# Kernel tuning notes

Measured on AMD Instinct MI355X. Metric: run time of the kernel, lower is better.

The kernel has to match this reference:

```python
import jax, jax.numpy as jnp
import numpy as np

S, T, H, D = 4096, 4096, 16, 64
N_EMBD = H * D

def setup_inputs() -> dict:
    key = jax.random.key(0)
    kq, kk, kv, kw = jax.random.split(key, 4)
    q = jax.random.normal(kq, (S, H, D), dtype=jnp.float32)
    k = jax.random.normal(kk, (T, H, D), dtype=jnp.float32)
    v = jax.random.normal(kv, (T, H, D), dtype=jnp.float32)
    # GPT-2 style init: std = 0.02 / sqrt(2 * n_layer), n_layer = 24
    W_proj = jax.random.normal(kw, (N_EMBD, N_EMBD), dtype=jnp.float32) * (0.02 / np.sqrt(2 * 24))
    return {"q": q, "k": k, "v": v, "W_proj": W_proj}

def reference(q, k, v, W_proj):
    s, h, d = q.shape
    t = k.shape[0]
    # causal bias: mask positions where query index < key index (future keys)
    causal_bias = (jnp.arange(s)[:, None] < jnp.arange(t)[None, :]).astype(jnp.float32) * -10000.0
    scale = 1.0 / jnp.sqrt(jnp.float32(d))
    # [h, s, t] scores in fp32 (matches original .astype(jnp.float32))
    scores = jnp.einsum('shd,thd->hst', q, k).astype(jnp.float32) * scale + causal_bias
    attn = jax.nn.softmax(scores, axis=-1).astype(q.dtype)
    # dropout p=0 / inference -> identity
    out = jnp.einsum('hst,thd->shd', attn, v).reshape(s, h * d)
    # nn.Linear (no bias) vmapped over tokens: y = x @ W.T
    return out @ W_proj.T
```

## Files before the change

### kernel.cpp

```cpp
#include <hip/hip_runtime.h>

#define S_LEN 4096
#define NH 16
#define DH 64
#define NE 1024

typedef __bf16 bf16_t;
typedef __bf16 bf16x8 __attribute__((ext_vector_type(8)));
typedef __bf16 bf16x4 __attribute__((ext_vector_type(4)));
typedef __bf16 bf16x2 __attribute__((ext_vector_type(2)));
typedef float  f32x4  __attribute__((ext_vector_type(4)));

#define QSCALE 0.180336879f

__global__ __launch_bounds__(256) void pack_all(const float* __restrict__ q,
                                                const float* __restrict__ k,
                                                const float* __restrict__ w,
                                                const float* __restrict__ v,
                                                bf16_t* __restrict__ qb,
                                                bf16_t* __restrict__ kb,
                                                bf16_t* __restrict__ wb,
                                                bf16_t* __restrict__ vt) {
    __shared__ bf16_t tile[64][65];
    const int bid = blockIdx.x;
    if (bid < 4096) {
        const int tid = bid * 256 + threadIdx.x;
        const int e = tid * 4;
        const int s = e >> 10;
        const int c = e & (NE - 1);
        const int h = c >> 6;
        const int d = c & (DH - 1);
        const int o = (h * S_LEN + s) * DH + d;
        float4 qv = *(const float4*)(q + e);
        float4 kv = *(const float4*)(k + e);
        bf16x4 qo, ko;
        qo[0] = (bf16_t)(qv.x * QSCALE); qo[1] = (bf16_t)(qv.y * QSCALE);
        qo[2] = (bf16_t)(qv.z * QSCALE); qo[3] = (bf16_t)(qv.w * QSCALE);
        ko[0] = (bf16_t)kv.x; ko[1] = (bf16_t)kv.y; ko[2] = (bf16_t)kv.z; ko[3] = (bf16_t)kv.w;
        *(bf16x4*)(qb + o) = qo;
        *(bf16x4*)(kb + o) = ko;
        if (tid < (NE * NE / 4)) {
            float4 wv = *(const float4*)(w + tid * 4);
            bf16x4 wo;
            wo[0] = (bf16_t)wv.x; wo[1] = (bf16_t)wv.y; wo[2] = (bf16_t)wv.z; wo[3] = (bf16_t)wv.w;
            *(bf16x4*)(wb + tid * 4) = wo;
        }
    } else {
        const int vb = bid - 4096;
        const int h  = vb >> 6;
        const int t0 = (vb & 63) * 64;
        const int r  = threadIdx.x >> 6;
        const int cl = threadIdx.x & 63;
#pragma unroll
        for (int rep = 0; rep < 16; ++rep) {
            int i = rep * 4 + r;
            tile[cl][i] = (bf16_t)v[(t0 + i) * NE + h * DH + cl];
        }
        __syncthreads();
        const int r2  = threadIdx.x >> 5;
        const int cl2 = (threadIdx.x & 31) * 2;
        const int np = (cl2 & 32) + ((cl2 >> 2) & 3) * 8 + ((cl2 >> 4) & 1) * 4 + (cl2 & 3);
#pragma unroll
        for (int rep = 0; rep < 8; ++rep) {
            int d = rep * 8 + r2;
            bf16x2 out;
            out[0] = tile[d][cl2];
            out[1] = tile[d][cl2 + 1];
            *(bf16x2*)(vt + (h * DH + d) * S_LEN + t0 + np) = out;
        }
    }
}

__global__ __launch_bounds__(512, 4) void attn(const bf16_t* __restrict__ qb,
                                               const bf16_t* __restrict__ kb,
                                               const bf16_t* __restrict__ vt,
                                               float* __restrict__ po,
                                               float* __restrict__ ls) {
    __shared__ __align__(16) bf16_t kbuf[2][64 * 72];
    __shared__ __align__(16) bf16_t vbuf[2][64 * 72];

    const int tid  = threadIdx.x;
    const int wave = tid >> 6;
    const int lane = tid & 63;
    const int l15  = lane & 15;
    const int quad = lane >> 4;
    const int h = blockIdx.x;
    const int x = blockIdx.y;

    const int sA = x;
    const int sB = 31 - x;
    const int n0 = x + 1;
    const int b1 = sB + 1;
    const int N  = 33;

    const bf16_t* __restrict__ qh = qb + h * (S_LEN * DH);
    const bf16_t* __restrict__ kh = kb + h * (S_LEN * DH);
    const bf16_t* __restrict__ vh = vt + h * (DH * S_LEN);

    const int row0 = tid >> 3;
    const int tc8  = (tid & 7) * 8;
    const int stg  = row0 * 72 + tc8;
    const int frg  = l15 * 72 + quad * 8;

    f32x4 o_acc[4];
    f32x4 rs;
    bf16x8 qA[2];
    bf16x8 ones;
#pragma unroll
    for (int e = 0; e < 8; ++e) ones[e] = (bf16_t)1.0f;
    int s0 = sA * 128 + wave * 16;

    auto load_q = [&](int s0_) {
#pragma unroll
        for (int dc = 0; dc < 2; ++dc)
            qA[dc] = *(const bf16x8*)(qh + (s0_ + l15) * DH + dc * 32 + quad * 8);
    };
    auto reset_acc = [&]() {
#pragma unroll
        for (int db = 0; db < 4; ++db) o_acc[db] = (f32x4){0.f, 0.f, 0.f, 0.f};
        rs = (f32x4){0.f, 0.f, 0.f, 0.f};
    };
    auto epilogue = [&](int s0_, int slot) {
        float* poz = po + (size_t)(slot * NH + h) * S_LEN * DH;
#pragma unroll
        for (int db = 0; db < 4; ++db)
#pragma unroll
            for (int r = 0; r < 4; ++r)
                poz[(s0_ + quad * 4 + r) * DH + db * 16 + l15] = o_acc[db][r];
        if (l15 == 0) {
            float* lsz = ls + (size_t)(slot * NH + h) * S_LEN;
#pragma unroll
            for (int r = 0; r < 4; ++r) lsz[s0_ + quad * 4 + r] = rs[r];
        }
    };

    load_q(s0);
    reset_acc();

    {
        bf16x8 kr = *(const bf16x8*)(kh + row0 * DH + tc8);
        bf16x8 vr = *(const bf16x8*)(vh + row0 * S_LEN + tc8);
        *(bf16x8*)(kbuf[0] + stg) = kr;
        *(bf16x8*)(vbuf[0] + stg) = vr;
    }
    __syncthreads();

#pragma unroll 2
    for (int j = 0; j < N; ++j) {
        if (j == n0) {
            epilogue(s0, 0);
            s0 = sB * 128 + wave * 16;
            load_q(s0);
            reset_acc();
        }
        const int t0 = (j < n0 ? j : b1 + (j - n0)) * 64;
        const bf16_t* kb_ = kbuf[j & 1];
        const bf16_t* vb_ = vbuf[j & 1];

        bf16x8 krn, vrn;
        const bool pf = (j + 1 < N);
        if (pf) {
            const int jn = j + 1;
            const int tn = (jn < n0 ? jn : b1 + (jn - n0)) * 64;
            krn = *(const bf16x8*)(kh + (tn + row0) * DH + tc8);
            vrn = *(const bf16x8*)(vh + row0 * S_LEN + tn + tc8);
        }

        if (t0 <= s0 + 15) {
            f32x4 c_[4];
#pragma unroll
            for (int ch = 0; ch < 4; ++ch) {
                bf16x8 kB0 = *(const bf16x8*)(kb_ + frg + ch * (16 * 72));
                bf16x8 kB1 = *(const bf16x8*)(kb_ + frg + ch * (16 * 72) + 32);
                f32x4 zr = (f32x4){0.f, 0.f, 0.f, 0.f};
                zr = __builtin_amdgcn_mfma_f32_16x16x32_bf16(kB0, qA[0], zr, 0, 0, 0);
                zr = __builtin_amdgcn_mfma_f32_16x16x32_bf16(kB1, qA[1], zr, 0, 0, 0);
                c_[ch] = zr;
            }

            const int query = s0 + l15;
            float p[4][4];
#pragma unroll
            for (int ch = 0; ch < 4; ++ch) {
                if (t0 + ch * 16 <= s0 + 15) {
                    const bool edge = (t0 + ch * 16 + 15 > s0);
#pragma unroll
                    for (int r = 0; r < 4; ++r) {
                        float cc = c_[ch][r];
                        if (edge) {
                            int key = t0 + ch * 16 + quad * 4 + r;
                            if (key > query) cc = -INFINITY;
                        }
                        p[ch][r] = exp2f(cc);
                    }
                } else {
#pragma unroll
                    for (int r = 0; r < 4; ++r) p[ch][r] = 0.0f;
                }
            }

            bf16x8 pA[2];
#pragma unroll
            for (int kc = 0; kc < 2; ++kc) {
                bf16x8 t;
                t[0] = (bf16_t)p[2 * kc][0];     t[1] = (bf16_t)p[2 * kc][1];
                t[2] = (bf16_t)p[2 * kc][2];     t[3] = (bf16_t)p[2 * kc][3];
                t[4] = (bf16_t)p[2 * kc + 1][0]; t[5] = (bf16_t)p[2 * kc + 1][1];
                t[6] = (bf16_t)p[2 * kc + 1][2]; t[7] = (bf16_t)p[2 * kc + 1][3];
                pA[kc] = t;
            }

            rs = __builtin_amdgcn_mfma_f32_16x16x32_bf16(pA[0], ones, rs, 0, 0, 0);
            rs = __builtin_amdgcn_mfma_f32_16x16x32_bf16(pA[1], ones, rs, 0, 0, 0);

#pragma unroll
            for (int db = 0; db < 4; ++db) {
#pragma unroll
                for (int kc = 0; kc < 2; ++kc) {
                    bf16x8 vB = *(const bf16x8*)(vb_ + frg + db * (16 * 72) + kc * 32);
                    o_acc[db] = __builtin_amdgcn_mfma_f32_16x16x32_bf16(pA[kc], vB, o_acc[db], 0, 0, 0);
                }
            }
        }

        if (pf) {
            *(bf16x8*)(kbuf[(j + 1) & 1] + stg) = krn;
            *(bf16x8*)(vbuf[(j + 1) & 1] + stg) = vrn;
        }
        __syncthreads();
    }

    epilogue(s0, 1);
}

__global__ __launch_bounds__(256) void combine(const float* __restrict__ po,
                                               const float* __restrict__ ls,
                                               bf16_t* __restrict__ xb) {
    const int idx = blockIdx.x * 256 + threadIdx.x;
    const int row = idx >> 8;
    const int c   = (idx & 255) * 4;
    const int h   = c >> 6;
    const int d   = c & 63;
    const size_t base0 = (size_t)(h) * S_LEN * DH + row * DH + d;
    const size_t base1 = (size_t)(NH + h) * S_LEN * DH + row * DH + d;
    float4 o0 = *(const float4*)(po + base0);
    float4 o1 = *(const float4*)(po + base1);
    float l = ls[(size_t)h * S_LEN + row] + ls[(size_t)(NH + h) * S_LEN + row];
    float inv = 1.0f / l;
    bf16x4 out;
    out[0] = (bf16_t)((o0.x + o1.x) * inv);
    out[1] = (bf16_t)((o0.y + o1.y) * inv);
    out[2] = (bf16_t)((o0.z + o1.z) * inv);
    out[3] = (bf16_t)((o0.w + o1.w) * inv);
    *(bf16x4*)(xb + (size_t)row * NE + c) = out;
}

__global__ __launch_bounds__(256, 4) void proj(const bf16_t* __restrict__ xb,
                                               const bf16_t* __restrict__ wb,
                                               float* __restrict__ y) {
    __shared__ __align__(16) bf16_t wbuf[2][64 * 72];
    const int tid  = threadIdx.x;
    const int wave = tid >> 6;
    const int lane = tid & 63;
    const int l15  = lane & 15;
    const int quad = lane >> 4;
    const int m0 = blockIdx.x * 64 + wave * 16;
    const int n0 = blockIdx.y * 64;

    const int row0 = tid >> 3;
    const int tc8  = (tid & 7) * 8;

    f32x4 acc[4];
#pragma unroll
    for (int nb = 0; nb < 4; ++nb) acc[nb] = (f32x4){0.f, 0.f, 0.f, 0.f};

    {
        bf16x8 wr0 = *(const bf16x8*)(wb + (n0 + row0) * NE + tc8);
        bf16x8 wr1 = *(const bf16x8*)(wb + (n0 + row0 + 32) * NE + tc8);
        *(bf16x8*)(wbuf[0] + row0 * 72 + tc8) = wr0;
        *(bf16x8*)(wbuf[0] + (row0 + 32) * 72 + tc8) = wr1;
    }
    bf16x8 a[2];
#pragma unroll
    for (int kc = 0; kc < 2; ++kc)
        a[kc] = *(const bf16x8*)(xb + (m0 + l15) * NE + kc * 32 + quad * 8);
    __syncthreads();

    for (int kt = 0; kt < 16; ++kt) {
        const bf16_t* wb_ = wbuf[kt & 1];
        const bool pf = (kt + 1 < 16);
        bf16x8 wr0, wr1, an[2];
        if (pf) {
            const int kn = (kt + 1) * 64;
            wr0 = *(const bf16x8*)(wb + (n0 + row0) * NE + kn + tc8);
            wr1 = *(const bf16x8*)(wb + (n0 + row0 + 32) * NE + kn + tc8);
#pragma unroll
            for (int kc = 0; kc < 2; ++kc)
                an[kc] = *(const bf16x8*)(xb + (m0 + l15) * NE + kn + kc * 32 + quad * 8);
        }

#pragma unroll
        for (int nb = 0; nb < 4; ++nb)
#pragma unroll
            for (int kc = 0; kc < 2; ++kc) {
                bf16x8 b = *(const bf16x8*)(wb_ + (nb * 16 + l15) * 72 + kc * 32 + quad * 8);
                acc[nb] = __builtin_amdgcn_mfma_f32_16x16x32_bf16(a[kc], b, acc[nb], 0, 0, 0);
            }

        if (pf) {
            *(bf16x8*)(wbuf[(kt + 1) & 1] + row0 * 72 + tc8) = wr0;
            *(bf16x8*)(wbuf[(kt + 1) & 1] + (row0 + 32) * 72 + tc8) = wr1;
#pragma unroll
            for (int kc = 0; kc < 2; ++kc) a[kc] = an[kc];
        }
        __syncthreads();
    }

#pragma unroll
    for (int nb = 0; nb < 4; ++nb)
#pragma unroll
        for (int r = 0; r < 4; ++r)
            y[(m0 + quad * 4 + r) * NE + n0 + nb * 16 + l15] = acc[nb][r];
}

extern "C" void kernel_launch(void* const* d_in, const int* in_sizes, int n_in,
                              void* d_out, int out_size, void* d_ws, size_t ws_size,
                              hipStream_t stream) {
    const float* q = (const float*)d_in[0];
    const float* k = (const float*)d_in[1];
    const float* v = (const float*)d_in[2];
    const float* w = (const float*)d_in[3];
    float* y = (float*)d_out;

    bf16_t* ws = (bf16_t*)d_ws;
    bf16_t* qb = ws;
    bf16_t* kb = qb + 4 * 1024 * 1024;
    bf16_t* vt = kb + 4 * 1024 * 1024;
    bf16_t* wb = vt + 4 * 1024 * 1024;
    bf16_t* xb = wb + 1024 * 1024;
    float*  po = (float*)(xb + 4 * 1024 * 1024);
    float*  ls = po + (size_t)2 * NH * S_LEN * DH;

    pack_all<<<dim3(4096 + 1024), dim3(256), 0, stream>>>(q, k, w, v, qb, kb, wb, vt);
    attn<<<dim3(NH, 32), dim3(512), 0, stream>>>(qb, kb, vt, po, ls);
    combine<<<dim3(4096), dim3(256), 0, stream>>>(po, ls, xb);
    proj<<<dim3(S_LEN / 64, NE / 64), dim3(256), 0, stream>>>(xb, wb, y);
}
```

Before: 196.3 us.

## Split paired causal query tiles into separate blocks via grid z dimension

Measured after the change: 221.0 us. 12.5% more time.

```diff
diff --git a/kernel.cpp b/kernel.cpp
--- a/kernel.cpp
+++ b/kernel.cpp
@@ -59,19 +59,20 @@
         __syncthreads();
         const int r2  = threadIdx.x >> 5;
         const int cl2 = (threadIdx.x & 31) * 2;
-        const int np = (cl2 & 32) + ((cl2 >> 2) & 3) * 8 + ((cl2 >> 4) & 1) * 4 + (cl2 & 3);
+        const int ip = (cl2 & 32) + ((cl2 >> 2) & 1) * 16 + ((cl2 >> 4) & 1) * 8 +
+                       ((cl2 >> 3) & 1) * 4 + (cl2 & 3);
 #pragma unroll
         for (int rep = 0; rep < 8; ++rep) {
             int d = rep * 8 + r2;
             bf16x2 out;
-            out[0] = tile[d][cl2];
-            out[1] = tile[d][cl2 + 1];
-            *(bf16x2*)(vt + (h * DH + d) * S_LEN + t0 + np) = out;
-        }
-    }
-}
-
-__global__ __launch_bounds__(512, 4) void attn(const bf16_t* __restrict__ qb,
+            out[0] = tile[d][ip];
+            out[1] = tile[d][ip + 1];
+            *(bf16x2*)(vt + (h * DH + d) * S_LEN + t0 + cl2) = out;
+        }
+    }
+}
+
+__global__ __launch_bounds__(512, 8) void attn(const bf16_t* __restrict__ qb,
                                                const bf16_t* __restrict__ kb,
                                                const bf16_t* __restrict__ vt,
                                                float* __restrict__ po,
@@ -86,6 +87,7 @@
     const int quad = lane >> 4;
     const int h = blockIdx.x;
     const int x = blockIdx.y;
+    const int z = blockIdx.z;
 
     const int sA = x;
     const int sB = 31 - x;
@@ -93,6 +95,10 @@
     const int b1 = sB + 1;
     const int N  = 33;
 
+    const int jb = z ? n0 : 0;
+    const int je = z ? N  : n0;
+    const int s0 = (z ? sB : sA) * 128 + wave * 16;
+
     const bf16_t* __restrict__ qh = qb + h * (S_LEN * DH);
     const bf16_t* __restrict__ kh = kb + h * (S_LEN * DH);
     const bf16_t* __restrict__ vh = vt + h * (DH * S_LEN);
@@ -108,60 +114,34 @@
     bf16x8 ones;
 #pragma unroll
     for (int e = 0; e < 8; ++e) ones[e] = (bf16_t)1.0f;
-    int s0 = sA * 128 + wave * 16;
-
-    auto load_q = [&](int s0_) {
-#pragma unroll
-        for (int dc = 0; dc < 2; ++dc)
-            qA[dc] = *(const bf16x8*)(qh + (s0_ + l15) * DH + dc * 32 + quad * 8);
-    };
-    auto reset_acc = [&]() {
-#pragma unroll
-        for (int db = 0; db < 4; ++db) o_acc[db] = (f32x4){0.f, 0.f, 0.f, 0.f};
-        rs = (f32x4){0.f, 0.f, 0.f, 0.f};
-    };
-    auto epilogue = [&](int s0_, int slot) {
-        float* poz = po + (size_t)(slot * NH + h) * S_LEN * DH;
-#pragma unroll
-        for (int db = 0; db < 4; ++db)
-#pragma unroll
-            for (int r = 0; r < 4; ++r)
-                poz[(s0_ + quad * 4 + r) * DH + db * 16 + l15] = o_acc[db][r];
-        if (l15 == 0) {
-            float* lsz = ls + (size_t)(slot * NH + h) * S_LEN;
-#pragma unroll
-            for (int r = 0; r < 4; ++r) lsz[s0_ + quad * 4 + r] = rs[r];
-        }
-    };
-
-    load_q(s0);
-    reset_acc();
+
+    auto t0_of = [&](int j) { return (j < n0 ? j : b1 + (j - n0)) * 64; };
+
+#pragma unroll
+    for (int dc = 0; dc < 2; ++dc)
+        qA[dc] = *(const bf16x8*)(qh + (s0 + l15) * DH + dc * 32 + quad * 8);
+#pragma unroll
+    for (int db = 0; db < 4; ++db) o_acc[db] = (f32x4){0.f, 0.f, 0.f, 0.f};
+    rs = (f32x4){0.f, 0.f, 0.f, 0.f};
 
     {
-        bf16x8 kr = *(const bf16x8*)(kh + row0 * DH + tc8);
-        bf16x8 vr = *(const bf16x8*)(vh + row0 * S_LEN + tc8);
-        *(bf16x8*)(kbuf[0] + stg) = kr;
-        *(bf16x8*)(vbuf[0] + stg) = vr;
+        const int t0 = t0_of(jb);
+        bf16x8 kr = *(const bf16x8*)(kh + (t0 + row0) * DH + tc8);
+        bf16x8 vr = *(const bf16x8*)(vh + row0 * S_LEN + t0 + tc8);
+        *(bf16x8*)(kbuf[jb & 1] + stg) = kr;
+        *(bf16x8*)(vbuf[jb & 1] + stg) = vr;
     }
     __syncthreads();
 
-#pragma unroll 2
-    for (int j = 0; j < N; ++j) {
-        if (j == n0) {
-            epilogue(s0, 0);
-            s0 = sB * 128 + wave * 16;
-            load_q(s0);
-            reset_acc();
-        }
-        const int t0 = (j < n0 ? j : b1 + (j - n0)) * 64;
+    for (int j = jb; j < je; ++j) {
+        const int t0 = t0_of(j);
         const bf16_t* kb_ = kbuf[j & 1];
         const bf16_t* vb_ = vbuf[j & 1];
 
         bf16x8 krn, vrn;
-        const bool pf = (j + 1 < N);
+        const bool pf = (j + 1 < je);
         if (pf) {
-            const int jn = j + 1;
-            const int tn = (jn < n0 ? jn : b1 + (jn - n0)) * 64;
+            const int tn = t0_of(j + 1);
             krn = *(const bf16x8*)(kh + (tn + row0) * DH + tc8);
             vrn = *(const bf16x8*)(vh + row0 * S_LEN + tn + tc8);
         }
@@ -230,7 +210,19 @@
         __syncthreads();
     }
 
-    epilogue(s0, 1);
+    {
+        float* poz = po + (size_t)(z * NH + h) * S_LEN * DH;
+#pragma unroll
+        for (int db = 0; db < 4; ++db)
+#pragma unroll
+            for (int r = 0; r < 4; ++r)
+                poz[(s0 + quad * 4 + r) * DH + db * 16 + l15] = o_acc[db][r];
+        if (l15 == 0) {
+            float* lsz = ls + (size_t)(z * NH + h) * S_LEN;
+#pragma unroll
+            for (int r = 0; r < 4; ++r) lsz[s0 + quad * 4 + r] = rs[r];
+        }
+    }
 }
 
 __global__ __launch_bounds__(256) void combine(const float* __restrict__ po,
@@ -342,7 +334,7 @@
     float*  ls = po + (size_t)2 * NH * S_LEN * DH;
 
     pack_all<<<dim3(4096 + 1024), dim3(256), 0, stream>>>(q, k, w, v, qb, kb, wb, vt);
-    attn<<<dim3(NH, 32), dim3(512), 0, stream>>>(qb, kb, vt, po, ls);
+    attn<<<dim3(NH, 32, 2), dim3(512), 0, stream>>>(qb, kb, vt, po, ls);
     combine<<<dim3(4096), dim3(256), 0, stream>>>(po, ls, xb);
     proj<<<dim3(S_LEN / 64, NE / 64), dim3(256), 0, stream>>>(xb, wb, y);
 }
```
